# Kernel tuning notes

Measured on AMD Instinct MI355X. Metric: run time of the kernel, lower is better.

## Reference

```python
import jax, jax.numpy as jnp
import numpy as np
import math

TWO_PI = 2.0 * math.pi
EPS = 1e-6


def _ffn(x, W1, b1, W2, b2):
    # x: [B, L, 1] -> [B, L, D]; Dense(relu) -> Dense(relu)
    h = jax.nn.relu(x @ W1 + b1)
    return jax.nn.relu(h @ W2 + b2)


def setup_inputs() -> dict:
    key = jax.random.key(0)
    ks = jax.random.split(key, 8)
    B, L, D = 4, 1024, 4
    t = jax.random.uniform(ks[0], (B, L), dtype=jnp.float32)  # timestamps
    def dense_init(k, fan_in, fan_out):
        lim = np.sqrt(6.0 / (fan_in + fan_out))
        return jax.random.uniform(k, (fan_in, fan_out), minval=-lim, maxval=lim, dtype=jnp.float32)
    inp = {"t": t}
    for name, k1, k2 in [("p", ks[1], ks[2]), ("s", ks[3], ks[4]), ("b", ks[5], ks[6])]:
        inp[f"W{name}1"] = dense_init(k1, 1, D)
        inp[f"b{name}1"] = jnp.zeros((D,), jnp.float32)
        inp[f"W{name}2"] = dense_init(k2, D, D)
        inp[f"b{name}2"] = jnp.zeros((D,), jnp.float32)
    return inp


def reference(t, Wp1, bp1, Wp2, bp2, Ws1, bs1, Ws2, bs2, Wb1, bb1, Wb2, bb2):
    x = t[..., None].astype(jnp.float32)  # [B, L, 1]

    # Periodic encoding: cos(2*pi*(p_q[i,d]*t_i - p_k[j,d]*t_j))
    pv = _ffn(x, Wp1, bp1, Wp2, bp2)          # [B, L, D]
    qp = TWO_PI * pv * x                       # [B, L, D]
    cos_enc = jnp.cos(qp[:, :, None, :] - qp[:, None, :, :])  # [B, Lq, Lk, D]

    # Gibbs encoding
    sg = _ffn(x, Ws1, bs1, Ws2, bs2)           # [B, L, D]
    sq = sg[:, :, None, :] + EPS               # [B, Lq, 1, D]
    sk = sg[:, None, :, :] + EPS               # [B, 1, Lk, D]
    denom = sq ** 2 + sk ** 2                  # [B, Lq, Lk, D]
    td2 = (t[:, :, None] - t[:, None, :]) ** 2  # [B, Lq, Lk]
    exp_enc = jnp.exp(-td2[..., None] / denom)
    local_enc = jnp.sqrt(2.0 * sq * sk / denom)
    gibbs_enc = local_enc * exp_enc

    # Basis expansion
    be = _ffn(x, Wb1, bb1, Wb2, bb2)           # [B, L, D]
    basis_qk = be[:, :, None, :] * be[:, None, :, :]  # [B, Lq, Lk, D]

    kernel = jnp.sum(basis_qk * gibbs_enc * cos_enc, axis=-1)  # [B, Lq, Lk]
    return kernel
```

## Files before the change

### kernel.cpp

```cpp
#include <hip/hip_runtime.h>

#define BB 4
#define LL 1024
#define TI 16

__device__ __forceinline__ void ffn4(float x,
    const float* __restrict__ W1, const float* __restrict__ b1,
    const float* __restrict__ W2, const float* __restrict__ b2, float out[4]) {
    float h[4];
#pragma unroll
    for (int d = 0; d < 4; ++d) h[d] = fmaxf(fmaf(x, W1[d], b1[d]), 0.0f);
#pragma unroll
    for (int j = 0; j < 4; ++j) {
        float a = b2[j];
#pragma unroll
        for (int d = 0; d < 4; ++d) a = fmaf(h[d], W2[d * 4 + j], a);
        out[j] = fmaxf(a, 0.0f);
    }
}

__device__ __forceinline__ void position_data(float x,
    const float* __restrict__ Wp1, const float* __restrict__ bp1,
    const float* __restrict__ Wp2, const float* __restrict__ bp2,
    const float* __restrict__ Ws1, const float* __restrict__ bs1,
    const float* __restrict__ Ws2, const float* __restrict__ bs2,
    const float* __restrict__ Wb1, const float* __restrict__ bb1,
    const float* __restrict__ Wb2, const float* __restrict__ bb2,
    float qc[4], float qs[4], float s2[4], float f[4])
{
    float pv[4], sg[4], bv[4];
    ffn4(x, Wp1, bp1, Wp2, bp2, pv);
    ffn4(x, Ws1, bs1, Ws2, bs2, sg);
    ffn4(x, Wb1, bb1, Wb2, bb2, bv);
#pragma unroll
    for (int d = 0; d < 4; ++d) {
        float qp = 6.283185307179586f * pv[d] * x;
        float s, c;
        __sincosf(qp, &s, &c);
        qc[d] = c; qs[d] = s;
        float sq = sg[d] + 1e-6f;
        s2[d] = sq * sq;
        f[d]  = bv[d] * sqrtf(sq);
    }
}

__global__ __launch_bounds__(256) void fused_kernel(const float* __restrict__ t,
    const float* __restrict__ Wp1, const float* __restrict__ bp1,
    const float* __restrict__ Wp2, const float* __restrict__ bp2,
    const float* __restrict__ Ws1, const float* __restrict__ bs1,
    const float* __restrict__ Ws2, const float* __restrict__ bs2,
    const float* __restrict__ Wb1, const float* __restrict__ bb1,
    const float* __restrict__ Wb2, const float* __restrict__ bb2,
    float* __restrict__ out)
{
    __shared__ float sh_t[TI];
    __shared__ float sh_qc[4][TI], sh_qs[4][TI], sh_s2[4][TI], sh_f[4][TI];

    const int tid = threadIdx.x;
    const int b   = blockIdx.z;
    const int i0  = blockIdx.y * TI;
    const int j   = blockIdx.x * 256 + tid;

    if (tid < TI) {
        float xi = t[b * LL + i0 + tid];
        float qc[4], qs[4], s2[4], f[4];
        position_data(xi, Wp1, bp1, Wp2, bp2, Ws1, bs1, Ws2, bs2,
                      Wb1, bb1, Wb2, bb2, qc, qs, s2, f);
        sh_t[tid] = xi;
#pragma unroll
        for (int d = 0; d < 4; ++d) {
            sh_qc[d][tid] = qc[d];
            sh_qs[d][tid] = qs[d];
            sh_s2[d][tid] = s2[d];
            sh_f[d][tid]  = f[d];
        }
    }

    const float xj = t[b * LL + j];
    float qcj[4], qsj[4], s2j[4], fj[4];
    position_data(xj, Wp1, bp1, Wp2, bp2, Ws1, bs1, Ws2, bs2,
                  Wb1, bb1, Wb2, bb2, qcj, qsj, s2j, fj);
#pragma unroll
    for (int d = 0; d < 4; ++d) fj[d] *= 1.41421356237309505f;

    __syncthreads();

    float* orow = out + ((size_t)b * LL + i0) * LL + j;

#pragma unroll 4
    for (int ii = 0; ii < TI; ++ii) {
        float td  = sh_t[ii] - xj;
        float td2 = td * td;
        float acc = 0.0f;
#pragma unroll
        for (int d = 0; d < 4; ++d) {
            float denom = sh_s2[d][ii] + s2j[d];
            float rs = rsqrtf(denom);
            float e  = __expf(-td2 * rs * rs);
            float cv = fmaf(sh_qc[d][ii], qcj[d], sh_qs[d][ii] * qsj[d]);
            acc = fmaf(sh_f[d][ii] * fj[d], rs * e * cv, acc);
        }
        orow[(size_t)ii * LL] = acc;
    }
}

extern "C" void kernel_launch(void* const* d_in, const int* in_sizes, int n_in,
                              void* d_out, int out_size, void* d_ws, size_t ws_size,
                              hipStream_t stream) {
    const float* t   = (const float*)d_in[0];
    const float* Wp1 = (const float*)d_in[1];
    const float* bp1 = (const float*)d_in[2];
    const float* Wp2 = (const float*)d_in[3];
    const float* bp2 = (const float*)d_in[4];
    const float* Ws1 = (const float*)d_in[5];
    const float* bs1 = (const float*)d_in[6];
    const float* Ws2 = (const float*)d_in[7];
    const float* bs2 = (const float*)d_in[8];
    const float* Wb1 = (const float*)d_in[9];
    const float* bb1 = (const float*)d_in[10];
    const float* Wb2 = (const float*)d_in[11];
    const float* bb2 = (const float*)d_in[12];
    float* out = (float*)d_out;

    dim3 grid(LL / 256, LL / TI, BB);
    hipLaunchKernelGGL(fused_kernel, grid, dim3(256), 0, stream,
                       t, Wp1, bp1, Wp2, bp2, Ws1, bs1, Ws2, bs2,
                       Wb1, bb1, Wb2, bb2, out);
}
```

Before: 18.30 us.

## Fold basis weights into cos/sin, process two columns per thread with packed math

Premultiplies the basis/sqrt factor into the cosine and sine terms per position, so the inner loop skips one multiply per dimension. Each thread now computes two adjacent output columns and writes a float2, which halves the grid and amortizes the shared-memory loads of row data. The per-dimension math uses 2-wide float vectors to encourage packed FP32 instructions, and row data is stored as f32x4 for vector LDS reads. This costs more registers per thread and fewer blocks, which could reduce latency hiding on a small, store-bound kernel.

After: 16.60 us. 9.3% less time.

```diff
diff --git a/kernel.cpp b/kernel.cpp
--- a/kernel.cpp
+++ b/kernel.cpp
@@ -3,6 +3,9 @@
 #define BB 4
 #define LL 1024
 #define TI 16
+
+typedef float f32x2 __attribute__((ext_vector_type(2)));
+typedef float f32x4 __attribute__((ext_vector_type(4)));
 
 __device__ __forceinline__ void ffn4(float x,
     const float* __restrict__ W1, const float* __restrict__ b1,
@@ -19,14 +22,15 @@
     }
 }
 
-__device__ __forceinline__ void position_data(float x,
+template<bool R2>
+__device__ __forceinline__ void posdata(float x,
     const float* __restrict__ Wp1, const float* __restrict__ bp1,
     const float* __restrict__ Wp2, const float* __restrict__ bp2,
     const float* __restrict__ Ws1, const float* __restrict__ bs1,
     const float* __restrict__ Ws2, const float* __restrict__ bs2,
     const float* __restrict__ Wb1, const float* __restrict__ bb1,
     const float* __restrict__ Wb2, const float* __restrict__ bb2,
-    float qc[4], float qs[4], float s2[4], float f[4])
+    f32x4& s2o, f32x4& co, f32x4& so)
 {
     float pv[4], sg[4], bv[4];
     ffn4(x, Wp1, bp1, Wp2, bp2, pv);
@@ -37,11 +41,28 @@
         float qp = 6.283185307179586f * pv[d] * x;
         float s, c;
         __sincosf(qp, &s, &c);
-        qc[d] = c; qs[d] = s;
         float sq = sg[d] + 1e-6f;
-        s2[d] = sq * sq;
-        f[d]  = bv[d] * sqrtf(sq);
+        float f  = bv[d] * sqrtf(sq);
+        if (R2) f *= 1.41421356237309505f;
+        s2o[d] = sq * sq;
+        co[d]  = f * c;
+        so[d]  = f * s;
     }
+}
+
+__device__ __forceinline__ f32x2 pair_term(f32x2 s2i, f32x2 s2j,
+                                           f32x2 ci, f32x2 cj,
+                                           f32x2 si, f32x2 sj,
+                                           f32x2 ntd2, f32x2 acc)
+{
+    f32x2 den = s2i + s2j;
+    f32x2 rs; rs.x = rsqrtf(den.x); rs.y = rsqrtf(den.y);
+    f32x2 rs2 = rs * rs;
+    f32x2 arg = ntd2 * rs2;
+    f32x2 e; e.x = __expf(arg.x); e.y = __expf(arg.y);
+    f32x2 cv = __builtin_elementwise_fma(ci, cj, si * sj);
+    f32x2 m = rs * e;
+    return __builtin_elementwise_fma(m, cv, acc);
 }
 
 __global__ __launch_bounds__(256) void fused_kernel(const float* __restrict__ t,
@@ -53,54 +74,65 @@
     const float* __restrict__ Wb2, const float* __restrict__ bb2,
     float* __restrict__ out)
 {
+    __shared__ f32x4 sh_s2[TI], sh_c[TI], sh_s[TI];
     __shared__ float sh_t[TI];
-    __shared__ float sh_qc[4][TI], sh_qs[4][TI], sh_s2[4][TI], sh_f[4][TI];
 
     const int tid = threadIdx.x;
     const int b   = blockIdx.z;
     const int i0  = blockIdx.y * TI;
-    const int j   = blockIdx.x * 256 + tid;
+    const int j0  = blockIdx.x * 512 + tid * 2;
 
     if (tid < TI) {
         float xi = t[b * LL + i0 + tid];
-        float qc[4], qs[4], s2[4], f[4];
-        position_data(xi, Wp1, bp1, Wp2, bp2, Ws1, bs1, Ws2, bs2,
-                      Wb1, bb1, Wb2, bb2, qc, qs, s2, f);
-        sh_t[tid] = xi;
-#pragma unroll
-        for (int d = 0; d < 4; ++d) {
-            sh_qc[d][tid] = qc[d];
-            sh_qs[d][tid] = qs[d];
-            sh_s2[d][tid] = s2[d];
-            sh_f[d][tid]  = f[d];
-        }
+        f32x4 s2i, ci, si;
+        posdata<true>(xi, Wp1, bp1, Wp2, bp2, Ws1, bs1, Ws2, bs2,
+                      Wb1, bb1, Wb2, bb2, s2i, ci, si);
+        sh_t[tid]  = xi;
+        sh_s2[tid] = s2i;
+        sh_c[tid]  = ci;
+        sh_s[tid]  = si;
     }
 
-    const float xj = t[b * LL + j];
-    float qcj[4], qsj[4], s2j[4], fj[4];
-    position_data(xj, Wp1, bp1, Wp2, bp2, Ws1, bs1, Ws2, bs2,
-                  Wb1, bb1, Wb2, bb2, qcj, qsj, s2j, fj);
-#pragma unroll
-    for (int d = 0; d < 4; ++d) fj[d] *= 1.41421356237309505f;
+    float tj0 = t[b * LL + j0];
+    float tj1 = t[b * LL + j0 + 1];
+    f32x4 s2j[2], cj[2], sj[2];
+    posdata<false>(tj0, Wp1, bp1, Wp2, bp2, Ws1, bs1, Ws2, bs2,
+                   Wb1, bb1, Wb2, bb2, s2j[0], cj[0], sj[0]);
+    posdata<false>(tj1, Wp1, bp1, Wp2, bp2, Ws1, bs1, Ws2, bs2,
+                   Wb1, bb1, Wb2, bb2, s2j[1], cj[1], sj[1]);
 
     __syncthreads();
 
-    float* orow = out + ((size_t)b * LL + i0) * LL + j;
+    float* obase = out + ((size_t)b * LL + i0) * LL + j0;
 
 #pragma unroll 4
     for (int ii = 0; ii < TI; ++ii) {
-        float td  = sh_t[ii] - xj;
-        float td2 = td * td;
-        float acc = 0.0f;
+        f32x4 s2i = sh_s2[ii], ci = sh_c[ii], si = sh_s[ii];
+        float tiv = sh_t[ii];
+        float res[2];
 #pragma unroll
-        for (int d = 0; d < 4; ++d) {
-            float denom = sh_s2[d][ii] + s2j[d];
-            float rs = rsqrtf(denom);
-            float e  = __expf(-td2 * rs * rs);
-            float cv = fmaf(sh_qc[d][ii], qcj[d], sh_qs[d][ii] * qsj[d]);
-            acc = fmaf(sh_f[d][ii] * fj[d], rs * e * cv, acc);
+        for (int jj = 0; jj < 2; ++jj) {
+            float td = tiv - (jj ? tj1 : tj0);
+            float n = -(td * td);
+            f32x2 ntd2; ntd2.x = n; ntd2.y = n;
+            f32x2 acc; acc.x = 0.0f; acc.y = 0.0f;
+            f32x2 s2i_lo; s2i_lo.x = s2i[0]; s2i_lo.y = s2i[1];
+            f32x2 s2i_hi; s2i_hi.x = s2i[2]; s2i_hi.y = s2i[3];
+            f32x2 ci_lo;  ci_lo.x  = ci[0];  ci_lo.y  = ci[1];
+            f32x2 ci_hi;  ci_hi.x  = ci[2];  ci_hi.y  = ci[3];
+            f32x2 si_lo;  si_lo.x  = si[0];  si_lo.y  = si[1];
+            f32x2 si_hi;  si_hi.x  = si[2];  si_hi.y  = si[3];
+            f32x2 s2j_lo; s2j_lo.x = s2j[jj][0]; s2j_lo.y = s2j[jj][1];
+            f32x2 s2j_hi; s2j_hi.x = s2j[jj][2]; s2j_hi.y = s2j[jj][3];
+            f32x2 cj_lo;  cj_lo.x  = cj[jj][0];  cj_lo.y  = cj[jj][1];
+            f32x2 cj_hi;  cj_hi.x  = cj[jj][2];  cj_hi.y  = cj[jj][3];
+            f32x2 sj_lo;  sj_lo.x  = sj[jj][0];  sj_lo.y  = sj[jj][1];
+            f32x2 sj_hi;  sj_hi.x  = sj[jj][2];  sj_hi.y  = sj[jj][3];
+            acc = pair_term(s2i_lo, s2j_lo, ci_lo, cj_lo, si_lo, sj_lo, ntd2, acc);
+            acc = pair_term(s2i_hi, s2j_hi, ci_hi, cj_hi, si_hi, sj_hi, ntd2, acc);
+            res[jj] = acc.x + acc.y;
         }
-        orow[(size_t)ii * LL] = acc;
+        *reinterpret_cast<float2*>(obase + (size_t)ii * LL) = make_float2(res[0], res[1]);
     }
 }
 
@@ -122,7 +154,7 @@
     const float* bb2 = (const float*)d_in[12];
     float* out = (float*)d_out;
 
-    dim3 grid(LL / 256, LL / TI, BB);
+    dim3 grid(LL / 512, LL / TI, BB);
     hipLaunchKernelGGL(fused_kernel, grid, dim3(256), 0, stream,
                        t, Wp1, bp1, Wp2, bp2, Ws1, bs1, Ws2, bs2,
                        Wb1, bb1, Wb2, bb2, out);
```

## Compute two output columns per thread with packed float2 math and exp2

Applied to the files above, without the earlier changes.

Each thread now produces two adjacent j outputs (JPT=2) with float2 stores, and the row tile shrinks from 16 to 8 rows. The f factor is folded into the cos/sin terms, per-row data is packed into an AoS shared struct, and the inner math uses packed f32x2 FMAs with exp2 and a precomputed -log2e scale. The aim is fewer instructions per output and wider stores. In exchange, the per-j position-data computation (three FFNs plus sincos) is amortized over only 8 rows instead of 16, and register use goes up.

Result: faster. 17.29 us (-5.5%).

```diff
diff --git a/kernel.cpp b/kernel.cpp
--- a/kernel.cpp
+++ b/kernel.cpp
@@ -2,7 +2,29 @@
 
 #define BB 4
 #define LL 1024
-#define TI 16
+#define TI 8
+#define JPT 2
+
+typedef float f32x2 __attribute__((ext_vector_type(2)));
+
+#define NEG_LOG2E -1.4426950408889634f
+#if __has_builtin(__builtin_amdgcn_exp2f)
+#define EXP2(x) __builtin_amdgcn_exp2f(x)
+#else
+#define EXP2(x) __expf((x) * 0.6931471805599453f)
+#endif
+
+struct PosData {
+    f32x2 s2l, s2h;
+    f32x2 cl,  ch;
+    f32x2 sl,  sh2;
+};
+
+struct PosRow {
+    PosData d;
+    float   tt;
+    float   pad;
+};
 
 __device__ __forceinline__ void ffn4(float x,
     const float* __restrict__ W1, const float* __restrict__ b1,
@@ -19,29 +41,51 @@
     }
 }
 
-__device__ __forceinline__ void position_data(float x,
+template<bool R2>
+__device__ __forceinline__ PosData posdata(float x,
     const float* __restrict__ Wp1, const float* __restrict__ bp1,
     const float* __restrict__ Wp2, const float* __restrict__ bp2,
     const float* __restrict__ Ws1, const float* __restrict__ bs1,
     const float* __restrict__ Ws2, const float* __restrict__ bs2,
     const float* __restrict__ Wb1, const float* __restrict__ bb1,
-    const float* __restrict__ Wb2, const float* __restrict__ bb2,
-    float qc[4], float qs[4], float s2[4], float f[4])
+    const float* __restrict__ Wb2, const float* __restrict__ bb2)
 {
     float pv[4], sg[4], bv[4];
     ffn4(x, Wp1, bp1, Wp2, bp2, pv);
     ffn4(x, Ws1, bs1, Ws2, bs2, sg);
     ffn4(x, Wb1, bb1, Wb2, bb2, bv);
+    float cc[4], ss[4], s2[4];
 #pragma unroll
     for (int d = 0; d < 4; ++d) {
         float qp = 6.283185307179586f * pv[d] * x;
         float s, c;
         __sincosf(qp, &s, &c);
-        qc[d] = c; qs[d] = s;
         float sq = sg[d] + 1e-6f;
+        float f  = bv[d] * sqrtf(sq);
+        if (R2) f *= 1.41421356237309505f;
         s2[d] = sq * sq;
-        f[d]  = bv[d] * sqrtf(sq);
+        cc[d] = f * c;
+        ss[d] = f * s;
     }
+    PosData r;
+    r.s2l = f32x2{s2[0], s2[1]}; r.s2h = f32x2{s2[2], s2[3]};
+    r.cl  = f32x2{cc[0], cc[1]}; r.ch  = f32x2{cc[2], cc[3]};
+    r.sl  = f32x2{ss[0], ss[1]}; r.sh2 = f32x2{ss[2], ss[3]};
+    return r;
+}
+
+__device__ __forceinline__ f32x2 pair_term(f32x2 s2i, f32x2 s2j,
+                                           f32x2 ci, f32x2 cj,
+                                           f32x2 si, f32x2 sj,
+                                           f32x2 ntd2l, f32x2 acc)
+{
+    f32x2 den = s2i + s2j;
+    f32x2 rs; rs.x = rsqrtf(den.x); rs.y = rsqrtf(den.y);
+    f32x2 rs2 = rs * rs;
+    f32x2 arg = ntd2l * rs2;
+    f32x2 e; e.x = EXP2(arg.x); e.y = EXP2(arg.y);
+    f32x2 cv = __builtin_elementwise_fma(ci, cj, si * sj);
+    return __builtin_elementwise_fma(rs * e, cv, acc);
 }
 
 __global__ __launch_bounds__(256) void fused_kernel(const float* __restrict__ t,
@@ -53,54 +97,50 @@
     const float* __restrict__ Wb2, const float* __restrict__ bb2,
     float* __restrict__ out)
 {
-    __shared__ float sh_t[TI];
-    __shared__ float sh_qc[4][TI], sh_qs[4][TI], sh_s2[4][TI], sh_f[4][TI];
+    __shared__ PosRow rows[TI];
 
     const int tid = threadIdx.x;
     const int b   = blockIdx.z;
     const int i0  = blockIdx.y * TI;
-    const int j   = blockIdx.x * 256 + tid;
+    const int j0  = blockIdx.x * (256 * JPT) + tid * JPT;
 
     if (tid < TI) {
         float xi = t[b * LL + i0 + tid];
-        float qc[4], qs[4], s2[4], f[4];
-        position_data(xi, Wp1, bp1, Wp2, bp2, Ws1, bs1, Ws2, bs2,
-                      Wb1, bb1, Wb2, bb2, qc, qs, s2, f);
-        sh_t[tid] = xi;
-#pragma unroll
-        for (int d = 0; d < 4; ++d) {
-            sh_qc[d][tid] = qc[d];
-            sh_qs[d][tid] = qs[d];
-            sh_s2[d][tid] = s2[d];
-            sh_f[d][tid]  = f[d];
-        }
+        rows[tid].d  = posdata<true>(xi, Wp1, bp1, Wp2, bp2, Ws1, bs1, Ws2, bs2,
+                                     Wb1, bb1, Wb2, bb2);
+        rows[tid].tt = xi;
     }
 
-    const float xj = t[b * LL + j];
-    float qcj[4], qsj[4], s2j[4], fj[4];
-    position_data(xj, Wp1, bp1, Wp2, bp2, Ws1, bs1, Ws2, bs2,
-                  Wb1, bb1, Wb2, bb2, qcj, qsj, s2j, fj);
+    float tj[JPT];
+    PosData jd[JPT];
 #pragma unroll
-    for (int d = 0; d < 4; ++d) fj[d] *= 1.41421356237309505f;
+    for (int jj = 0; jj < JPT; ++jj) {
+        tj[jj] = t[b * LL + j0 + jj];
+        jd[jj] = posdata<false>(tj[jj], Wp1, bp1, Wp2, bp2, Ws1, bs1, Ws2, bs2,
+                                Wb1, bb1, Wb2, bb2);
+    }
 
     __syncthreads();
 
-    float* orow = out + ((size_t)b * LL + i0) * LL + j;
+    float* obase = out + ((size_t)b * LL + i0) * LL + j0;
 
-#pragma unroll 4
+#pragma unroll
     for (int ii = 0; ii < TI; ++ii) {
-        float td  = sh_t[ii] - xj;
-        float td2 = td * td;
-        float acc = 0.0f;
+        PosRow rw = rows[ii];
+        float res[JPT];
 #pragma unroll
-        for (int d = 0; d < 4; ++d) {
-            float denom = sh_s2[d][ii] + s2j[d];
-            float rs = rsqrtf(denom);
-            float e  = __expf(-td2 * rs * rs);
-            float cv = fmaf(sh_qc[d][ii], qcj[d], sh_qs[d][ii] * qsj[d]);
-            acc = fmaf(sh_f[d][ii] * fj[d], rs * e * cv, acc);
+        for (int jj = 0; jj < JPT; ++jj) {
+            float td = rw.tt - tj[jj];
+            float n  = td * td * NEG_LOG2E;
+            f32x2 ntd2l; ntd2l.x = n; ntd2l.y = n;
+            f32x2 acc; acc.x = 0.0f; acc.y = 0.0f;
+            acc = pair_term(rw.d.s2l, jd[jj].s2l, rw.d.cl, jd[jj].cl,
+                            rw.d.sl,  jd[jj].sl,  ntd2l, acc);
+            acc = pair_term(rw.d.s2h, jd[jj].s2h, rw.d.ch, jd[jj].ch,
+                            rw.d.sh2, jd[jj].sh2, ntd2l, acc);
+            res[jj] = acc.x + acc.y;
         }
-        orow[(size_t)ii * LL] = acc;
+        *reinterpret_cast<float2*>(obase + (size_t)ii * LL) = make_float2(res[0], res[1]);
     }
 }
 
@@ -122,7 +162,7 @@
     const float* bb2 = (const float*)d_in[12];
     float* out = (float*)d_out;
 
-    dim3 grid(LL / 256, LL / TI, BB);
+    dim3 grid(LL / (256 * JPT), LL / TI, BB);
     hipLaunchKernelGGL(fused_kernel, grid, dim3(256), 0, stream,
                        t, Wp1, bp1, Wp2, bp2, Ws1, bs1, Ws2, bs2,
                        Wb1, bb1, Wb2, bb2, out);
```

## Split per-position FFN precompute into separate kernel and vectorize pair kernel

Applied to the files above, without the earlier changes.

Moves the three tiny FFNs, sincos and sqrt per position into a separate precompute kernel that writes packed float4 arrays to workspace, so the pair kernel no longer recomputes them once per block. The f factor is folded into the cos/sin terms, exp is replaced with exp2 using a prescaled log2e argument, and each thread now computes two columns with float2 stores over TI=8 rows. This adds a second kernel launch and a workspace round trip, and it assumes the workspace is large enough.

New measurement: 19.98 us. +9.2%, slower.

```diff
diff --git a/kernel.cpp b/kernel.cpp
--- a/kernel.cpp
+++ b/kernel.cpp
@@ -2,7 +2,18 @@
 
 #define BB 4
 #define LL 1024
-#define TI 16
+#define NPOS (BB*LL)
+#define TI 8
+#define JPT 2
+
+typedef float f32x4 __attribute__((ext_vector_type(4)));
+
+#define NEG_LOG2E -1.4426950408889634f
+#if __has_builtin(__builtin_amdgcn_exp2f)
+#define EXP2(x) __builtin_amdgcn_exp2f(x)
+#else
+#define EXP2(x) __expf((x) * 0.6931471805599453f)
+#endif
 
 __device__ __forceinline__ void ffn4(float x,
     const float* __restrict__ W1, const float* __restrict__ b1,
@@ -19,88 +30,92 @@
     }
 }
 
-__device__ __forceinline__ void position_data(float x,
+__global__ void precompute_kernel(const float* __restrict__ t,
     const float* __restrict__ Wp1, const float* __restrict__ bp1,
     const float* __restrict__ Wp2, const float* __restrict__ bp2,
     const float* __restrict__ Ws1, const float* __restrict__ bs1,
     const float* __restrict__ Ws2, const float* __restrict__ bs2,
     const float* __restrict__ Wb1, const float* __restrict__ bb1,
     const float* __restrict__ Wb2, const float* __restrict__ bb2,
-    float qc[4], float qs[4], float s2[4], float f[4])
+    f32x4* __restrict__ S2, f32x4* __restrict__ C, f32x4* __restrict__ S)
 {
+    int p = blockIdx.x * blockDim.x + threadIdx.x;
+    if (p >= NPOS) return;
+    float x = t[p];
     float pv[4], sg[4], bv[4];
     ffn4(x, Wp1, bp1, Wp2, bp2, pv);
     ffn4(x, Ws1, bs1, Ws2, bs2, sg);
     ffn4(x, Wb1, bb1, Wb2, bb2, bv);
+    f32x4 s2o, co, so;
 #pragma unroll
     for (int d = 0; d < 4; ++d) {
         float qp = 6.283185307179586f * pv[d] * x;
         float s, c;
         __sincosf(qp, &s, &c);
-        qc[d] = c; qs[d] = s;
         float sq = sg[d] + 1e-6f;
-        s2[d] = sq * sq;
-        f[d]  = bv[d] * sqrtf(sq);
+        float f  = bv[d] * sqrtf(sq);
+        s2o[d] = sq * sq;
+        co[d]  = f * c;
+        so[d]  = f * s;
     }
+    S2[p] = s2o; C[p] = co; S[p] = so;
 }
 
-__global__ __launch_bounds__(256) void fused_kernel(const float* __restrict__ t,
-    const float* __restrict__ Wp1, const float* __restrict__ bp1,
-    const float* __restrict__ Wp2, const float* __restrict__ bp2,
-    const float* __restrict__ Ws1, const float* __restrict__ bs1,
-    const float* __restrict__ Ws2, const float* __restrict__ bs2,
-    const float* __restrict__ Wb1, const float* __restrict__ bb1,
-    const float* __restrict__ Wb2, const float* __restrict__ bb2,
-    float* __restrict__ out)
+__device__ __forceinline__ float dot_term(f32x4 s2i, f32x4 s2j,
+                                          f32x4 ci, f32x4 cj,
+                                          f32x4 si, f32x4 sj, float ntd2l)
 {
+    f32x4 den = s2i + s2j;
+    f32x4 rs;
+#pragma unroll
+    for (int k = 0; k < 4; ++k) rs[k] = rsqrtf(den[k]);
+    f32x4 arg = (ntd2l * rs) * rs;
+    f32x4 e;
+#pragma unroll
+    for (int k = 0; k < 4; ++k) e[k] = EXP2(arg[k]);
+    f32x4 cv = __builtin_elementwise_fma(ci, cj, si * sj);
+    f32x4 m = (rs * e) * cv;
+    return (m.x + m.y) + (m.z + m.w);
+}
+
+__global__ __launch_bounds__(256) void pair_kernel(const float* __restrict__ t,
+    const f32x4* __restrict__ S2, const f32x4* __restrict__ C,
+    const f32x4* __restrict__ S, float* __restrict__ out)
+{
+    __shared__ f32x4 sh_s2[TI], sh_c[TI], sh_s[TI];
     __shared__ float sh_t[TI];
-    __shared__ float sh_qc[4][TI], sh_qs[4][TI], sh_s2[4][TI], sh_f[4][TI];
 
     const int tid = threadIdx.x;
     const int b   = blockIdx.z;
     const int i0  = blockIdx.y * TI;
-    const int j   = blockIdx.x * 256 + tid;
+    const int j0  = blockIdx.x * (256 * JPT) + tid * JPT;
 
     if (tid < TI) {
-        float xi = t[b * LL + i0 + tid];
-        float qc[4], qs[4], s2[4], f[4];
-        position_data(xi, Wp1, bp1, Wp2, bp2, Ws1, bs1, Ws2, bs2,
-                      Wb1, bb1, Wb2, bb2, qc, qs, s2, f);
-        sh_t[tid] = xi;
-#pragma unroll
-        for (int d = 0; d < 4; ++d) {
-            sh_qc[d][tid] = qc[d];
-            sh_qs[d][tid] = qs[d];
-            sh_s2[d][tid] = s2[d];
-            sh_f[d][tid]  = f[d];
-        }
+        int p = b * LL + i0 + tid;
+        sh_s2[tid] = S2[p];
+        sh_c[tid]  = C[p] * 1.41421356237309505f;
+        sh_s[tid]  = S[p] * 1.41421356237309505f;
+        sh_t[tid]  = t[p];
     }
 
-    const float xj = t[b * LL + j];
-    float qcj[4], qsj[4], s2j[4], fj[4];
-    position_data(xj, Wp1, bp1, Wp2, bp2, Ws1, bs1, Ws2, bs2,
-                  Wb1, bb1, Wb2, bb2, qcj, qsj, s2j, fj);
-#pragma unroll
-    for (int d = 0; d < 4; ++d) fj[d] *= 1.41421356237309505f;
+    const int pj = b * LL + j0;
+    float tj0 = t[pj], tj1 = t[pj + 1];
+    f32x4 s2j0 = S2[pj], s2j1 = S2[pj + 1];
+    f32x4 cj0  = C[pj],  cj1  = C[pj + 1];
+    f32x4 sj0  = S[pj],  sj1  = S[pj + 1];
 
     __syncthreads();
 
-    float* orow = out + ((size_t)b * LL + i0) * LL + j;
+    float* obase = out + ((size_t)b * LL + i0) * LL + j0;
 
-#pragma unroll 4
+#pragma unroll
     for (int ii = 0; ii < TI; ++ii) {
-        float td  = sh_t[ii] - xj;
-        float td2 = td * td;
-        float acc = 0.0f;
-#pragma unroll
-        for (int d = 0; d < 4; ++d) {
-            float denom = sh_s2[d][ii] + s2j[d];
-            float rs = rsqrtf(denom);
-            float e  = __expf(-td2 * rs * rs);
-            float cv = fmaf(sh_qc[d][ii], qcj[d], sh_qs[d][ii] * qsj[d]);
-            acc = fmaf(sh_f[d][ii] * fj[d], rs * e * cv, acc);
-        }
-        orow[(size_t)ii * LL] = acc;
+        f32x4 s2i = sh_s2[ii], ci = sh_c[ii], si = sh_s[ii];
+        float tiv = sh_t[ii];
+        float td0 = tiv - tj0, td1 = tiv - tj1;
+        float r0 = dot_term(s2i, s2j0, ci, cj0, si, sj0, td0 * td0 * NEG_LOG2E);
+        float r1 = dot_term(s2i, s2j1, ci, cj1, si, sj1, td1 * td1 * NEG_LOG2E);
+        *reinterpret_cast<float2*>(obase + (size_t)ii * LL) = make_float2(r0, r1);
     }
 }
 
@@ -122,8 +137,15 @@
     const float* bb2 = (const float*)d_in[12];
     float* out = (float*)d_out;
 
-    dim3 grid(LL / 256, LL / TI, BB);
-    hipLaunchKernelGGL(fused_kernel, grid, dim3(256), 0, stream,
+    f32x4* S2 = (f32x4*)d_ws;
+    f32x4* C  = S2 + NPOS;
+    f32x4* S  = C + NPOS;
+
+    hipLaunchKernelGGL(precompute_kernel, dim3(NPOS / 64), dim3(64), 0, stream,
                        t, Wp1, bp1, Wp2, bp2, Ws1, bs1, Ws2, bs2,
-                       Wb1, bb1, Wb2, bb2, out);
+                       Wb1, bb1, Wb2, bb2, S2, C, S);
+
+    dim3 grid(LL / (256 * JPT), LL / TI, BB);
+    hipLaunchKernelGGL(pair_kernel, grid, dim3(256), 0, stream,
+                       t, S2, C, S, out);
 }
```
